# Kernel tuning notes

Hardware: AMD Instinct MI355X
Metric: run time of the kernel (lower is better)

Reference implementation:

```python
import jax, jax.numpy as jnp
import numpy as np

HIDDEN = 4096
N_HEADS = 32
N_KV_HEADS = 8
HEAD_DIM = HIDDEN // N_HEADS  # 128
ROPE_THETA = 10000.0
NEG_INF = -1e9


def rotate_half(x):
    x1, x2 = jnp.split(x, 2, axis=-1)
    return jnp.concatenate([-x2, x1], axis=-1)


def rope_cos_sin(seq_len, dim, dtype):
    inv_freq = 1.0 / (ROPE_THETA ** (jnp.arange(0, dim, 2, dtype=jnp.float32) / dim))
    t = jnp.arange(seq_len, dtype=jnp.float32)
    freqs = jnp.outer(t, inv_freq)              # (S, dim/2)
    emb = jnp.concatenate([freqs, freqs], -1)   # (S, dim)
    return jnp.cos(emb).astype(dtype), jnp.sin(emb).astype(dtype)


def setup_inputs() -> dict:
    key = jax.random.key(0)
    ks = jax.random.split(key, 5)
    B, S = 2, 2048
    hidden_states = jax.random.normal(ks[0], (B, S, HIDDEN), jnp.float32)
    # additive causal mask (B, 1, S, S)
    causal = jnp.triu(jnp.full((S, S), NEG_INF, jnp.float32), k=1)
    attention_mask = jnp.broadcast_to(causal[None, None], (B, 1, S, S))
    scale = 0.02
    wq = jax.random.normal(ks[1], (HIDDEN, HIDDEN), jnp.float32) * scale
    wk = jax.random.normal(ks[2], (N_KV_HEADS * HEAD_DIM, HIDDEN), jnp.float32) * scale
    wv = jax.random.normal(ks[3], (N_KV_HEADS * HEAD_DIM, HIDDEN), jnp.float32) * scale
    wo = jax.random.normal(ks[4], (HIDDEN, HIDDEN), jnp.float32) * scale
    return {"hidden_states": hidden_states, "attention_mask": attention_mask,
            "wq": wq, "wk": wk, "wv": wv, "wo": wo}


def reference(hidden_states, attention_mask, wq, wk, wv, wo):
    B, S, _ = hidden_states.shape
    H, Hk, D = N_HEADS, N_KV_HEADS, HEAD_DIM
    G = H // Hk  # kv groups

    q = (hidden_states @ wq.T).reshape(B, S, H, D).transpose(0, 2, 1, 3)   # (B,H,S,D)
    k = (hidden_states @ wk.T).reshape(B, S, Hk, D).transpose(0, 2, 1, 3)  # (B,Hk,S,D)
    v = (hidden_states @ wv.T).reshape(B, S, Hk, D).transpose(0, 2, 1, 3)

    cos, sin = rope_cos_sin(S, D, hidden_states.dtype)  # (S,D)
    cos = cos[None, None]  # (1,1,S,D)
    sin = sin[None, None]
    q = q * cos + rotate_half(q) * sin
    k = k * cos + rotate_half(k) * sin

    # GQA without materializing repeated K/V: view q as (B,Hk,G,S,D)
    qg = q.reshape(B, Hk, G, S, D)
    scores = jnp.einsum('bkgqd,bkld->bkgql', qg, k) / jnp.sqrt(jnp.asarray(D, q.dtype))
    scores = scores + attention_mask[:, :, None]  # (B,1,1,S,S) broadcast
    attn = jax.nn.softmax(scores.astype(jnp.float32), axis=-1).astype(q.dtype)
    out = jnp.einsum('bkgql,bkld->bkgqd', attn, v)  # (B,Hk,G,S,D)
    out = out.reshape(B, H, S, D).transpose(0, 2, 1, 3).reshape(B, S, H * D)
    return out @ wo.T
```

## Files before the change

### kernel.cpp

```cpp
#include <hip/hip_runtime.h>
#include <hip/hip_bf16.h>
#include <stdint.h>


#define HIDDEN 4096
#define NH 32
#define NKV 8
#define HD 128
#define SLEN 2048
#define BATCH 2
#define QKVLD 6144

typedef __attribute__((ext_vector_type(8))) short bf16x8;
typedef __attribute__((ext_vector_type(4))) float f32x4;

__device__ __forceinline__ unsigned short f2bf(float f) {
  __hip_bfloat16 h = __float2bfloat16(f);
  return *reinterpret_cast<unsigned short*>(&h);
}
__device__ __forceinline__ float bf2f(unsigned short h) {
  union { uint32_t u; float f; } v; v.u = ((uint32_t)h) << 16;
  return v.f;
}
__device__ __forceinline__ void gload_lds16(const void* g, void* l) {
  __builtin_amdgcn_global_load_lds(
      (const __attribute__((address_space(1))) unsigned int*)g,
      (__attribute__((address_space(3))) unsigned int*)l, 16, 0, 0);
}

__global__ __launch_bounds__(256) void cvt_f32_bf16(const float* __restrict__ in,
                                                    unsigned short* __restrict__ out) {
  size_t i = ((size_t)blockIdx.x * 256 + threadIdx.x) * 8;
  f32x4 a = *(const f32x4*)&in[i];
  f32x4 b = *(const f32x4*)&in[i + 4];
  bf16x8 o;
#pragma unroll
  for (int j = 0; j < 4; ++j) { o[j] = (short)f2bf(a[j]); o[4 + j] = (short)f2bf(b[j]); }
  *(bf16x8*)&out[i] = o;
}

__device__ __forceinline__ void store_out(unsigned short* C, size_t i, float v) { C[i] = f2bf(v); }
__device__ __forceinline__ void store_out(float* C, size_t i, float v) { C[i] = v; }

template <typename OutT>
__global__ __launch_bounds__(512, 2)
void gemm_bt256(const unsigned short* __restrict__ A, const unsigned short* __restrict__ B,
                OutT* __restrict__ C, int M, int N, int K) {
  __shared__ __align__(16) unsigned short lds[4 * 2048 * 8];

  const int tid = threadIdx.x;
  const int lane = tid & 63, w = tid >> 6;
  const int lr = lane & 15, lg = lane >> 4;
  const int wr = w >> 2, wc = w & 3;

  const int nbn = N >> 8;
  const int nwg = gridDim.x;
  int wg = (int)blockIdx.x;
  wg = (wg & 7) * (nwg >> 3) + (wg >> 3);
  const int bm = wg / nbn, bn = wg % nbn;

  const unsigned short* Ab = A + (size_t)bm * 256 * K;
  const unsigned short* Bb = B + (size_t)bn * 256 * K;

  f32x4 acc[8][4] = {};

  auto stage = [&](int t2) {
    const int kt = t2 * 32;
    unsigned short* lb = lds + (size_t)(t2 & 3) * 2048 * 8;
#pragma unroll
    for (int j = 0; j < 2; ++j) {
      int idx = tid + j * 512;
      gload_lds16(Ab + (size_t)(idx >> 2) * K + kt + (idx & 3) * 8,
                  lb + (size_t)(w * 64 + j * 512) * 8);
    }
#pragma unroll
    for (int j = 0; j < 2; ++j) {
      int idx = tid + j * 512;
      gload_lds16(Bb + (size_t)(idx >> 2) * K + kt + (idx & 3) * 8,
                  lb + (size_t)(1024 + w * 64 + j * 512) * 8);
    }
  };

  const int NT = K >> 5;

  stage(0);
  stage(1);
  stage(2);
  asm volatile("s_waitcnt vmcnt(8)" ::: "memory");
  __builtin_amdgcn_s_barrier();
  asm volatile("" ::: "memory");

#pragma unroll 1
  for (int t = 0; t < NT; ++t) {
    if (t + 3 < NT) stage(t + 3);

    const unsigned short* bufp = lds + (size_t)(t & 3) * 2048 * 8;
    bf16x8 af[8], bfv[4];
#pragma unroll
    for (int mi = 0; mi < 8; ++mi)
      af[mi] = *(const bf16x8*)&bufp[(size_t)(wr * 512 + mi * 64 + lr * 4 + lg) * 8];
#pragma unroll
    for (int ni = 0; ni < 4; ++ni)
      bfv[ni] = *(const bf16x8*)&bufp[(size_t)(1024 + wc * 256 + ni * 64 + lr * 4 + lg) * 8];

    __builtin_amdgcn_s_setprio(1);
#pragma unroll
    for (int mi = 0; mi < 8; ++mi)
#pragma unroll
      for (int ni = 0; ni < 4; ++ni)
        acc[mi][ni] = __builtin_amdgcn_mfma_f32_16x16x32_bf16(af[mi], bfv[ni], acc[mi][ni], 0, 0, 0);
    __builtin_amdgcn_s_setprio(0);

    if (t + 1 < NT) {
      if (t + 3 < NT)      asm volatile("s_waitcnt vmcnt(8)" ::: "memory");
      else if (t + 2 < NT) asm volatile("s_waitcnt vmcnt(4)" ::: "memory");
      else                 asm volatile("s_waitcnt vmcnt(0)" ::: "memory");
      __builtin_amdgcn_s_barrier();
      asm volatile("" ::: "memory");
    }
  }

#pragma unroll
  for (int mi = 0; mi < 8; ++mi)
#pragma unroll
    for (int ni = 0; ni < 4; ++ni)
#pragma unroll
      for (int r = 0; r < 4; ++r) {
        size_t row = (size_t)bm * 256 + wr * 128 + mi * 16 + lg * 4 + r;
        size_t col = (size_t)bn * 256 + wc * 64 + ni * 16 + lr;
        store_out(C, row * N + col, acc[mi][ni][r]);
      }
}

__global__ __launch_bounds__(256) void rope_tables(float* __restrict__ ct, float* __restrict__ st) {
  int idx = blockIdx.x * 256 + threadIdx.x;
  int s = idx >> 6, j = idx & 63;
  float inv = exp2f(-(float)j * (13.287712379549449f / 64.f));
  float f = (float)s * inv;
  ct[idx] = cosf(f);
  st[idx] = sinf(f);
}

__global__ __launch_bounds__(256) void rope_apply(unsigned short* __restrict__ X, int ld,
                                                  const float* __restrict__ ct,
                                                  const float* __restrict__ st, int heads) {
  int idx = blockIdx.x * 256 + threadIdx.x;
  int jc = (idx & 7) * 8;
  int t2 = idx >> 3;
  int hh = t2 % heads;
  int row = t2 / heads;
  int s = row & (SLEN - 1);
  unsigned short* p = X + (size_t)row * ld + hh * HD;
  bf16x8 lo = *(bf16x8*)&p[jc];
  bf16x8 hi = *(bf16x8*)&p[64 + jc];
  bf16x8 nlo, nhi;
#pragma unroll
  for (int j = 0; j < 8; ++j) {
    float c = ct[s * 64 + jc + j];
    float sn = st[s * 64 + jc + j];
    float xl = bf2f((unsigned short)(lo[j]));
    float xh = bf2f((unsigned short)(hi[j]));
    nlo[j] = (short)f2bf(xl * c - xh * sn);
    nhi[j] = (short)f2bf(xh * c + xl * sn);
  }
  *(bf16x8*)&p[jc] = nlo;
  *(bf16x8*)&p[64 + jc] = nhi;
}

__global__ __launch_bounds__(256) void transpose_v(const unsigned short* __restrict__ Vsrc, int ld,
                                                   unsigned short* __restrict__ VT) {
  __shared__ unsigned short tile[64][66];
  const int t = threadIdx.x;
  const int bs = blockIdx.x;
  const int bd = blockIdx.y;
  const int b = bs >> 5;
  const int s0 = (bs & 31) * 64;
  const int d0 = bd * 64;
#pragma unroll
  for (int it = 0; it < 2; ++it) {
    int si = (t >> 3) + it * 32;
    int dj = (t & 7) * 8;
    bf16x8 v = *(const bf16x8*)&Vsrc[(size_t)(b * SLEN + s0 + si) * ld + d0 + dj];
#pragma unroll
    for (int j = 0; j < 8; ++j) tile[si][dj + j] = (unsigned short)(v[j]);
  }
  __syncthreads();
#pragma unroll
  for (int it = 0; it < 2; ++it) {
    int di = (t >> 3) + it * 32;
    int sj = (t & 7) * 8;
    bf16x8 o;
#pragma unroll
    for (int j = 0; j < 8; ++j) o[j] = (short)tile[sj + j][di];
    int c = d0 + di;
    int kvh = c >> 7, d = c & 127;
    *(bf16x8*)&VT[(((size_t)b * NKV + kvh) * HD + d) * SLEN + s0 + sj] = o;
  }
}

__global__ __launch_bounds__(256, 2)
void attn_fwd(const unsigned short* __restrict__ QKV, const unsigned short* __restrict__ VTm,
              unsigned short* __restrict__ Om) {
  const int blk = blockIdx.x;
  const int xcd = blk & 7, jj = blk >> 3;
  const int g = xcd + ((jj >> 5) << 3);
  const int pair = jj & 31;
  const int kvh = g & 7, b = g >> 3;
  const int tid = threadIdx.x;
  const int lane = tid & 63, w = tid >> 6;
  const int lr = lane & 15, lg = lane >> 4;
  const int h = kvh * 4 + w;

  __shared__ __align__(16) unsigned short Ksm[64 * 136];
  __shared__ __align__(16) unsigned short Vsm[128 * 72];
  __shared__ __align__(16) unsigned short Psm[4][32 * 72];
  __shared__ float Alds[4][32];

  const float SL2E = 0.1275378504229740f;

  const unsigned short* Kb0 = QKV + (size_t)(b * SLEN) * QKVLD + 4096 + kvh * HD;
  const unsigned short* VTb = VTm + ((size_t)(b * NKV + kvh) * HD) * SLEN;

#pragma unroll 1
  for (int halfq = 0; halfq < 2; ++halfq) {
    const int qt = halfq ? (63 - pair) : pair;
    const int q0 = qt * 32;
    const int ntiles = (qt >> 1) + 1;

    bf16x8 qf[2][4];
    const unsigned short* Qb = QKV + (size_t)(b * SLEN + q0) * QKVLD + h * HD;
#pragma unroll
    for (int ni = 0; ni < 2; ++ni)
#pragma unroll
      for (int kd = 0; kd < 4; ++kd)
        qf[ni][kd] = *(const bf16x8*)&Qb[(size_t)(ni * 16 + lr) * QKVLD + kd * 32 + lg * 8];

    f32x4 acc_o[2][8] = {};
    float m_run[2] = {-1e30f, -1e30f};
    float l_run[2] = {0.f, 0.f};

    bf16x8 kreg[4], vreg[4];
#pragma unroll
    for (int i = 0; i < 4; ++i) {
      int c = tid + i * 256;
      kreg[i] = *(const bf16x8*)&Kb0[(size_t)(c >> 4) * QKVLD + (c & 15) * 8];
      vreg[i] = *(const bf16x8*)&VTb[(size_t)(c >> 3) * SLEN + (c & 7) * 8];
    }

#pragma unroll 1
    for (int t = 0; t < ntiles; ++t) {
      const int kv0 = t * 64;
      __syncthreads();
#pragma unroll
      for (int i = 0; i < 4; ++i) {
        int c = tid + i * 256;
        *(bf16x8*)&Ksm[(c >> 4) * 136 + (c & 15) * 8] = kreg[i];
        *(bf16x8*)&Vsm[(c >> 3) * 72 + (c & 7) * 8] = vreg[i];
      }
      __syncthreads();

      if (t + 1 < ntiles) {
#pragma unroll
        for (int i = 0; i < 4; ++i) {
          int c = tid + i * 256;
          kreg[i] = *(const bf16x8*)&Kb0[(size_t)(kv0 + 64 + (c >> 4)) * QKVLD + (c & 15) * 8];
          vreg[i] = *(const bf16x8*)&VTb[(size_t)(c >> 3) * SLEN + kv0 + 64 + (c & 7) * 8];
        }
      }

      f32x4 accs[4][2] = {};
#pragma unroll
      for (int kd = 0; kd < 4; ++kd) {
        bf16x8 kf[4];
#pragma unroll
        for (int mi = 0; mi < 4; ++mi)
          kf[mi] = *(const bf16x8*)&Ksm[(mi * 16 + lr) * 136 + kd * 32 + lg * 8];
        __builtin_amdgcn_s_setprio(1);
#pragma unroll
        for (int mi = 0; mi < 4; ++mi)
#pragma unroll
          for (int ni = 0; ni < 2; ++ni)
            accs[mi][ni] =
                __builtin_amdgcn_mfma_f32_16x16x32_bf16(kf[mi], qf[ni][kd], accs[mi][ni], 0, 0, 0);
        __builtin_amdgcn_s_setprio(0);
      }

      const bool domask = (t == ntiles - 1);
      float alpha[2];
#pragma unroll
      for (int ni = 0; ni < 2; ++ni) {
        float cmax = -1e30f;
#pragma unroll
        for (int mi = 0; mi < 4; ++mi)
#pragma unroll
          for (int r = 0; r < 4; ++r) {
            float s = accs[mi][ni][r] * SL2E;
            if (domask) {
              int key = kv0 + mi * 16 + lg * 4 + r;
              int qq = q0 + ni * 16 + lr;
              if (key > qq) s = -1e30f;
            }
            accs[mi][ni][r] = s;
            cmax = fmaxf(cmax, s);
          }
        cmax = fmaxf(cmax, __shfl_xor(cmax, 16));
        cmax = fmaxf(cmax, __shfl_xor(cmax, 32));
        float mnew = fmaxf(m_run[ni], cmax);
        alpha[ni] = exp2f(m_run[ni] - mnew);
        float psum = 0.f;
#pragma unroll
        for (int mi = 0; mi < 4; ++mi)
#pragma unroll
          for (int r = 0; r < 4; ++r) {
            float p = exp2f(accs[mi][ni][r] - mnew);
            accs[mi][ni][r] = p;
            psum += p;
          }
        psum += __shfl_xor(psum, 16);
        psum += __shfl_xor(psum, 32);
        l_run[ni] = l_run[ni] * alpha[ni] + psum;
        m_run[ni] = mnew;
      }

      if (__any(alpha[0] < 1.f) || __any(alpha[1] < 1.f)) {
        if (lg == 0) { Alds[w][lr] = alpha[0]; Alds[w][16 + lr] = alpha[1]; }
        f32x4 al0 = *(const f32x4*)&Alds[w][lg * 4];
        f32x4 al1 = *(const f32x4*)&Alds[w][16 + lg * 4];
#pragma unroll
        for (int nd = 0; nd < 8; ++nd)
#pragma unroll
          for (int r = 0; r < 4; ++r) {
            acc_o[0][nd][r] *= al0[r];
            acc_o[1][nd][r] *= al1[r];
          }
      }

#pragma unroll
      for (int ni = 0; ni < 2; ++ni)
#pragma unroll
        for (int mi = 0; mi < 4; ++mi)
#pragma unroll
          for (int rp = 0; rp < 4; rp += 2) {
            uint32_t pk = (uint32_t)f2bf(accs[mi][ni][rp]) |
                          ((uint32_t)f2bf(accs[mi][ni][rp + 1]) << 16);
            *(uint32_t*)&Psm[w][(ni * 16 + lr) * 72 + mi * 16 + lg * 4 + rp] = pk;
          }

#pragma unroll
      for (int ks = 0; ks < 2; ++ks) {
        bf16x8 pa[2];
#pragma unroll
        for (int pm = 0; pm < 2; ++pm)
          pa[pm] = *(const bf16x8*)&Psm[w][(pm * 16 + lr) * 72 + ks * 32 + lg * 8];
        __builtin_amdgcn_s_setprio(1);
#pragma unroll
        for (int nd = 0; nd < 8; ++nd) {
          bf16x8 vb = *(const bf16x8*)&Vsm[(nd * 16 + lr) * 72 + ks * 32 + lg * 8];
#pragma unroll
          for (int pm = 0; pm < 2; ++pm)
            acc_o[pm][nd] =
                __builtin_amdgcn_mfma_f32_16x16x32_bf16(pa[pm], vb, acc_o[pm][nd], 0, 0, 0);
        }
        __builtin_amdgcn_s_setprio(0);
      }
    }

    if (lg == 0) {
      Alds[w][lr] = 1.f / l_run[0];
      Alds[w][16 + lr] = 1.f / l_run[1];
    }
    f32x4 li0 = *(const f32x4*)&Alds[w][lg * 4];
    f32x4 li1 = *(const f32x4*)&Alds[w][16 + lg * 4];
    unsigned short* Ob = Om + ((size_t)(b * SLEN + q0) * NH + h) * HD;
#pragma unroll
    for (int pm = 0; pm < 2; ++pm)
#pragma unroll
      for (int nd = 0; nd < 8; ++nd)
#pragma unroll
        for (int r = 0; r < 4; ++r) {
          int qq = pm * 16 + lg * 4 + r;
          float v = acc_o[pm][nd][r] * (pm ? li1[r] : li0[r]);
          Ob[(size_t)qq * (NH * HD) + nd * 16 + lr] = f2bf(v);
        }
  }
}

extern "C" void kernel_launch(void* const* d_in, const int* in_sizes, int n_in,
                              void* d_out, int out_size, void* d_ws, size_t ws_size,
                              hipStream_t stream) {
  const float* hidden = (const float*)d_in[0];
  const float* wq = (const float*)d_in[2];
  const float* wk = (const float*)d_in[3];
  const float* wv = (const float*)d_in[4];
  const float* wo = (const float*)d_in[5];

  char* ws = (char*)d_ws;
  const size_t MB = 1ull << 20;
  unsigned short* Xbf  = (unsigned short*)(ws);
  unsigned short* Wqkv = (unsigned short*)(ws + 32 * MB);
  unsigned short* QKV  = (unsigned short*)(ws + 80 * MB);
  unsigned short* Ob   = (unsigned short*)(ws + 128 * MB);
  unsigned short* VTb  = (unsigned short*)(ws + 160 * MB);
  float* ct = (float*)(ws + 168 * MB);
  float* st = (float*)(ws + 168 * MB + 524288);

  cvt_f32_bf16<<<8192, 256, 0, stream>>>(hidden, Xbf);
  cvt_f32_bf16<<<8192, 256, 0, stream>>>(wq, Wqkv);
  cvt_f32_bf16<<<2048, 256, 0, stream>>>(wk, Wqkv + (size_t)4096 * 4096);
  cvt_f32_bf16<<<2048, 256, 0, stream>>>(wv, Wqkv + (size_t)5120 * 4096);

  gemm_bt256<unsigned short><<<384, 512, 0, stream>>>(Xbf, Wqkv, QKV, 4096, 6144, 4096);

  rope_tables<<<512, 256, 0, stream>>>(ct, st);
  rope_apply<<<4096, 256, 0, stream>>>(QKV, QKVLD, ct, st, NH);
  rope_apply<<<1024, 256, 0, stream>>>(QKV + 4096, QKVLD, ct, st, NKV);

  transpose_v<<<dim3(64, 16), 256, 0, stream>>>(QKV + 5120, QKVLD, VTb);

  attn_fwd<<<512, 256, 0, stream>>>(QKV, VTb, Ob);

  cvt_f32_bf16<<<8192, 256, 0, stream>>>(wo, Wqkv);
  gemm_bt256<float><<<256, 512, 0, stream>>>(Ob, Wqkv, (float*)d_out, 4096, 4096, 4096);
}
```

Measured before the change: 601.1 us.

## Restructure GEMM main loop into four interleaved phases with swizzled double-buffered LDS

Rewrites the 256x256 bf16 GEMM main loop to use 64-wide K tiles in two LDS buffers, split into four phases that each issue LDS reads, one half-tile global prefetch and 16 MFMAs, separated by barriers. It also XOR-swizzles the LDS column layout to reduce bank conflicts on fragment reads. The goal is better overlap of global loads, LDS reads and MFMA work, and lower register pressure from holding fewer A fragments at once. The cost is more barriers per iteration and a more fragile vmcnt accounting scheme.

```diff
diff --git a/kernel.cpp b/kernel.cpp
--- a/kernel.cpp
+++ b/kernel.cpp
@@ -46,12 +46,13 @@
 __global__ __launch_bounds__(512, 2)
 void gemm_bt256(const unsigned short* __restrict__ A, const unsigned short* __restrict__ B,
                 OutT* __restrict__ C, int M, int N, int K) {
-  __shared__ __align__(16) unsigned short lds[4 * 2048 * 8];
+  __shared__ __align__(16) unsigned short lds[2 * 4096 * 8];
 
   const int tid = threadIdx.x;
   const int lane = tid & 63, w = tid >> 6;
   const int lr = lane & 15, lg = lane >> 4;
   const int wr = w >> 2, wc = w & 3;
+  const int rsw = (lr >> 1) & 3;
 
   const int nbn = N >> 8;
   const int nwg = gridDim.x;
@@ -64,60 +65,87 @@
 
   f32x4 acc[8][4] = {};
 
-  auto stage = [&](int t2) {
-    const int kt = t2 * 32;
-    unsigned short* lb = lds + (size_t)(t2 & 3) * 2048 * 8;
+  auto stage_half = [&](int isA, int ks, int tile) {
+    const unsigned short* gb = isA ? Ab : Bb;
+    const int rb = (tile & 1) * 4096 + (isA ? 0 : 2048) + ks * 1024;
+    const int kcol = tile * 64 + ks * 32;
 #pragma unroll
     for (int j = 0; j < 2; ++j) {
-      int idx = tid + j * 512;
-      gload_lds16(Ab + (size_t)(idx >> 2) * K + kt + (idx & 3) * 8,
-                  lb + (size_t)(w * 64 + j * 512) * 8);
-    }
-#pragma unroll
-    for (int j = 0; j < 2; ++j) {
-      int idx = tid + j * 512;
-      gload_lds16(Bb + (size_t)(idx >> 2) * K + kt + (idx & 3) * 8,
-                  lb + (size_t)(1024 + w * 64 + j * 512) * 8);
+      int L = tid + j * 512;
+      int row = L >> 2, cc = L & 3;
+      int scc = cc ^ ((row >> 1) & 3);
+      gload_lds16(gb + (size_t)row * K + kcol + scc * 8, lds + (size_t)(rb + L) * 8);
     }
   };
-
-  const int NT = K >> 5;
-
-  stage(0);
-  stage(1);
-  stage(2);
-  asm volatile("s_waitcnt vmcnt(8)" ::: "memory");
+  auto read_a4 = [&](bf16x8* dst, int ks, int mi0, int p) {
+#pragma unroll
+    for (int i = 0; i < 4; ++i) {
+      int row = wr * 128 + (mi0 + i) * 16 + lr;
+      dst[i] = *(const bf16x8*)&lds[(size_t)(p * 4096 + ks * 1024 + row * 4 + (lg ^ rsw)) * 8];
+    }
+  };
+  auto read_b4 = [&](bf16x8* dst, int ks, int p) {
+#pragma unroll
+    for (int i = 0; i < 4; ++i) {
+      int row = wc * 64 + i * 16 + lr;
+      dst[i] =
+          *(const bf16x8*)&lds[(size_t)(p * 4096 + 2048 + ks * 1024 + row * 4 + (lg ^ rsw)) * 8];
+    }
+  };
+
+#define PHASE_SYNC()                                    \
+  __builtin_amdgcn_s_barrier();                         \
+  asm volatile("s_waitcnt lgkmcnt(0)" ::: "memory");    \
+  __builtin_amdgcn_sched_barrier(0)
+
+#define MFMA16(afq, bq, mb)                                                                   \
+  __builtin_amdgcn_s_setprio(1);                                                              \
+  _Pragma("unroll") for (int i_ = 0; i_ < 4; ++i_) _Pragma("unroll") for (int n_ = 0; n_ < 4; \
+                                                                          ++n_) acc[mb + i_]  \
+      [n_] = __builtin_amdgcn_mfma_f32_16x16x32_bf16(afq[i_], bq[n_], acc[mb + i_][n_], 0, 0, 0); \
+  __builtin_amdgcn_s_setprio(0);                                                              \
+  __builtin_amdgcn_s_barrier()
+
+  const int NT = K >> 6;
+
+  stage_half(1, 0, 0); stage_half(0, 0, 0); stage_half(1, 1, 0); stage_half(0, 1, 0);
+  if (NT > 1) { stage_half(0, 0, 1); stage_half(1, 0, 1); stage_half(0, 1, 1); }
+  if (NT > 1) asm volatile("s_waitcnt vmcnt(6)" ::: "memory");
+  else        asm volatile("s_waitcnt vmcnt(0)" ::: "memory");
   __builtin_amdgcn_s_barrier();
   asm volatile("" ::: "memory");
 
 #pragma unroll 1
   for (int t = 0; t < NT; ++t) {
-    if (t + 3 < NT) stage(t + 3);
-
-    const unsigned short* bufp = lds + (size_t)(t & 3) * 2048 * 8;
-    bf16x8 af[8], bfv[4];
-#pragma unroll
-    for (int mi = 0; mi < 8; ++mi)
-      af[mi] = *(const bf16x8*)&bufp[(size_t)(wr * 512 + mi * 64 + lr * 4 + lg) * 8];
-#pragma unroll
-    for (int ni = 0; ni < 4; ++ni)
-      bfv[ni] = *(const bf16x8*)&bufp[(size_t)(1024 + wc * 256 + ni * 64 + lr * 4 + lg) * 8];
-
-    __builtin_amdgcn_s_setprio(1);
-#pragma unroll
-    for (int mi = 0; mi < 8; ++mi)
-#pragma unroll
-      for (int ni = 0; ni < 4; ++ni)
-        acc[mi][ni] = __builtin_amdgcn_mfma_f32_16x16x32_bf16(af[mi], bfv[ni], acc[mi][ni], 0, 0, 0);
-    __builtin_amdgcn_s_setprio(0);
-
-    if (t + 1 < NT) {
-      if (t + 3 < NT)      asm volatile("s_waitcnt vmcnt(8)" ::: "memory");
-      else if (t + 2 < NT) asm volatile("s_waitcnt vmcnt(4)" ::: "memory");
-      else                 asm volatile("s_waitcnt vmcnt(0)" ::: "memory");
-      __builtin_amdgcn_s_barrier();
-      asm volatile("" ::: "memory");
-    }
+    const int p = t & 1;
+    bf16x8 afq[4], afq2[4], bq0[4], bq1[4];
+
+    read_a4(afq, 0, 0, p);
+    read_b4(bq0, 0, p);
+    if (t + 1 < NT) stage_half(1, 1, t + 1);
+    PHASE_SYNC();
+    MFMA16(afq, bq0, 0);
+
+    read_a4(afq2, 0, 4, p);
+    if (t + 2 < NT) stage_half(0, 0, t + 2);
+    PHASE_SYNC();
+    MFMA16(afq2, bq0, 4);
+
+    read_a4(afq, 1, 0, p);
+    read_b4(bq1, 1, p);
+    if (t + 2 < NT) stage_half(1, 0, t + 2);
+    PHASE_SYNC();
+    MFMA16(afq, bq1, 0);
+
+    read_a4(afq2, 1, 4, p);
+    if (t + 2 < NT) stage_half(0, 1, t + 2);
+    PHASE_SYNC();
+    MFMA16(afq2, bq1, 4);
+
+    if (t + 2 < NT)      asm volatile("s_waitcnt vmcnt(6)" ::: "memory");
+    else if (t + 1 < NT) asm volatile("s_waitcnt vmcnt(0)" ::: "memory");
+    __builtin_amdgcn_s_barrier();
+    asm volatile("" ::: "memory");
   }
 
 #pragma unroll
@@ -130,6 +158,8 @@
         size_t col = (size_t)bn * 256 + wc * 64 + ni * 16 + lr;
         store_out(C, row * N + col, acc[mi][ni][r]);
       }
+#undef PHASE_SYNC
+#undef MFMA16
 }
 
 __global__ __launch_bounds__(256) void rope_tables(float* __restrict__ ct, float* __restrict__ st) {
```

Measured after the change: 590.3 us. About the same (-1.8%).

## Restructure GEMM mainloop into 64-wide K tiles with phased double-buffered LDS pipeline

Applied to the files above, without the earlier changes.

Rewrites the bf16 GEMM main loop to use 64-wide K tiles in a two-buffer LDS layout. Each tile is split into four phases that interleave LDS reads, async global-to-LDS staging of later sub-tiles, and 16-MFMA groups, separated by barriers. An XOR swizzle on the LDS chunk index is added to reduce bank conflicts on fragment reads. The aim is finer overlap of memory and MFMA work, at the cost of more barriers per K step and more complex waitcnt bookkeeping.

```diff
diff --git a/kernel.cpp b/kernel.cpp
--- a/kernel.cpp
+++ b/kernel.cpp
@@ -46,12 +46,13 @@
 __global__ __launch_bounds__(512, 2)
 void gemm_bt256(const unsigned short* __restrict__ A, const unsigned short* __restrict__ B,
                 OutT* __restrict__ C, int M, int N, int K) {
-  __shared__ __align__(16) unsigned short lds[4 * 2048 * 8];
+  __shared__ __align__(16) unsigned short lds[2 * 4096 * 8];
 
   const int tid = threadIdx.x;
   const int lane = tid & 63, w = tid >> 6;
   const int lr = lane & 15, lg = lane >> 4;
   const int wr = w >> 2, wc = w & 3;
+  const int rsw = (lr >> 1) & 3;
 
   const int nbn = N >> 8;
   const int nwg = gridDim.x;
@@ -62,62 +63,97 @@
   const unsigned short* Ab = A + (size_t)bm * 256 * K;
   const unsigned short* Bb = B + (size_t)bn * 256 * K;
 
+  const int r0 = tid >> 2, s0 = (tid & 3) ^ ((tid >> 3) & 3);
+  const int L1 = tid + 512;
+  const int r1 = L1 >> 2, s1 = (L1 & 3) ^ ((L1 >> 3) & 3);
+  const unsigned short* gA0 = Ab + (size_t)r0 * K + s0 * 8;
+  const unsigned short* gA1 = Ab + (size_t)r1 * K + s1 * 8;
+  const unsigned short* gB0 = Bb + (size_t)r0 * K + s0 * 8;
+  const unsigned short* gB1 = Bb + (size_t)r1 * K + s1 * 8;
+
+  const unsigned short* rdA0 = &lds[(size_t)(wr * 512 + lr * 4 + (lg ^ rsw)) * 8];
+  const unsigned short* rdA1 = rdA0 + 32768;
+  const unsigned short* rdB0 = &lds[(size_t)(2048 + wc * 256 + lr * 4 + (lg ^ rsw)) * 8];
+  const unsigned short* rdB1 = rdB0 + 32768;
+
   f32x4 acc[8][4] = {};
 
-  auto stage = [&](int t2) {
-    const int kt = t2 * 32;
-    unsigned short* lb = lds + (size_t)(t2 & 3) * 2048 * 8;
-#pragma unroll
-    for (int j = 0; j < 2; ++j) {
-      int idx = tid + j * 512;
-      gload_lds16(Ab + (size_t)(idx >> 2) * K + kt + (idx & 3) * 8,
-                  lb + (size_t)(w * 64 + j * 512) * 8);
-    }
-#pragma unroll
-    for (int j = 0; j < 2; ++j) {
-      int idx = tid + j * 512;
-      gload_lds16(Bb + (size_t)(idx >> 2) * K + kt + (idx & 3) * 8,
-                  lb + (size_t)(1024 + w * 64 + j * 512) * 8);
-    }
+  auto stageA = [&](int ks, int tile) {
+    unsigned short* d = &lds[(size_t)((tile & 1) * 4096 + ks * 1024 + tid) * 8];
+    const int off = tile * 64 + ks * 32;
+    gload_lds16(gA0 + off, d);
+    gload_lds16(gA1 + off, d + 4096);
   };
-
-  const int NT = K >> 5;
-
-  stage(0);
-  stage(1);
-  stage(2);
-  asm volatile("s_waitcnt vmcnt(8)" ::: "memory");
+  auto stageB = [&](int ks, int tile) {
+    unsigned short* d = &lds[(size_t)((tile & 1) * 4096 + 2048 + ks * 1024 + tid) * 8];
+    const int off = tile * 64 + ks * 32;
+    gload_lds16(gB0 + off, d);
+    gload_lds16(gB1 + off, d + 4096);
+  };
+
+  const int NT = K >> 6;
+
+#define PHASE_SYNC()                                  \
+  __builtin_amdgcn_s_barrier();                       \
+  asm volatile("s_waitcnt lgkmcnt(0)" ::: "memory");  \
+  __builtin_amdgcn_sched_barrier(0)
+
+#define MFMA16(afq, bq, mb)                                                       \
+  __builtin_amdgcn_s_setprio(1);                                                  \
+  _Pragma("unroll") for (int i_ = 0; i_ < 4; ++i_)                                \
+  _Pragma("unroll") for (int n_ = 0; n_ < 4; ++n_)                                \
+    acc[(mb) + i_][n_] = __builtin_amdgcn_mfma_f32_16x16x32_bf16(                 \
+        afq[i_], bq[n_], acc[(mb) + i_][n_], 0, 0, 0);                            \
+  __builtin_amdgcn_s_setprio(0)
+
+#define RD_A(dst, P, ks, mi0)                                                     \
+  _Pragma("unroll") for (int i_ = 0; i_ < 4; ++i_)                                \
+    dst[i_] = *(const bf16x8*)((P ? rdA1 : rdA0) + (ks) * 8192 + ((mi0) + i_) * 512)
+#define RD_B(dst, P, ks)                                                          \
+  _Pragma("unroll") for (int i_ = 0; i_ < 4; ++i_)                                \
+    dst[i_] = *(const bf16x8*)((P ? rdB1 : rdB0) + (ks) * 8192 + i_ * 512)
+
+#define TILE_BODY(P, t)                                                           \
+  {                                                                               \
+    bf16x8 a0[4], a1[4], b0[4], b1[4];                                            \
+                     \
+    RD_A(a0, P, 0, 0); RD_B(b0, P, 0);                                            \
+    if ((t) + 1 < NT) stageA(1, (t) + 1);                                         \
+    PHASE_SYNC();                                                                 \
+    MFMA16(a0, b0, 0);                                                            \
+    __builtin_amdgcn_s_barrier();                                                 \
+                            \
+    RD_A(a1, P, 0, 4);                                                            \
+    if ((t) + 2 < NT) stageB(0, (t) + 2);                                         \
+    PHASE_SYNC();                                                                 \
+    MFMA16(a1, b0, 4);                                                            \
+    __builtin_amdgcn_s_barrier();                                                 \
+                     \
+    RD_A(a0, P, 1, 0); RD_B(b1, P, 1);                                            \
+    if ((t) + 2 < NT) stageA(0, (t) + 2);                                         \
+    PHASE_SYNC();                                                                 \
+    MFMA16(a0, b1, 0);                                                            \
+    __builtin_amdgcn_s_barrier();                                                 \
+            \
+    RD_A(a1, P, 1, 4);                                                            \
+    if ((t) + 2 < NT) stageB(1, (t) + 2);                                         \
+    PHASE_SYNC();                                                                 \
+    MFMA16(a1, b1, 4);                                                            \
+    if ((t) + 2 < NT)      asm volatile("s_waitcnt vmcnt(6)" ::: "memory");       \
+    else if ((t) + 1 < NT) asm volatile("s_waitcnt vmcnt(0)" ::: "memory");       \
+    __builtin_amdgcn_s_barrier();                                                 \
+  }
+
+  stageA(0, 0); stageB(0, 0); stageA(1, 0); stageB(1, 0);
+  stageB(0, 1); stageA(0, 1); stageB(1, 1);
+  asm volatile("s_waitcnt vmcnt(6)" ::: "memory");
   __builtin_amdgcn_s_barrier();
   asm volatile("" ::: "memory");
 
 #pragma unroll 1
-  for (int t = 0; t < NT; ++t) {
-    if (t + 3 < NT) stage(t + 3);
-
-    const unsigned short* bufp = lds + (size_t)(t & 3) * 2048 * 8;
-    bf16x8 af[8], bfv[4];
-#pragma unroll
-    for (int mi = 0; mi < 8; ++mi)
-      af[mi] = *(const bf16x8*)&bufp[(size_t)(wr * 512 + mi * 64 + lr * 4 + lg) * 8];
-#pragma unroll
-    for (int ni = 0; ni < 4; ++ni)
-      bfv[ni] = *(const bf16x8*)&bufp[(size_t)(1024 + wc * 256 + ni * 64 + lr * 4 + lg) * 8];
-
-    __builtin_amdgcn_s_setprio(1);
-#pragma unroll
-    for (int mi = 0; mi < 8; ++mi)
-#pragma unroll
-      for (int ni = 0; ni < 4; ++ni)
-        acc[mi][ni] = __builtin_amdgcn_mfma_f32_16x16x32_bf16(af[mi], bfv[ni], acc[mi][ni], 0, 0, 0);
-    __builtin_amdgcn_s_setprio(0);
-
-    if (t + 1 < NT) {
-      if (t + 3 < NT)      asm volatile("s_waitcnt vmcnt(8)" ::: "memory");
-      else if (t + 2 < NT) asm volatile("s_waitcnt vmcnt(4)" ::: "memory");
-      else                 asm volatile("s_waitcnt vmcnt(0)" ::: "memory");
-      __builtin_amdgcn_s_barrier();
-      asm volatile("" ::: "memory");
-    }
+  for (int t = 0; t < NT; t += 2) {
+    TILE_BODY(0, t);
+    TILE_BODY(1, t + 1);
   }
 
 #pragma unroll
@@ -130,6 +166,11 @@
         size_t col = (size_t)bn * 256 + wc * 64 + ni * 16 + lr;
         store_out(C, row * N + col, acc[mi][ni][r]);
       }
+#undef PHASE_SYNC
+#undef MFMA16
+#undef RD_A
+#undef RD_B
+#undef TILE_BODY
 }
 
 __global__ __launch_bounds__(256) void rope_tables(float* __restrict__ ct, float* __restrict__ st) {
@@ -409,7 +450,7 @@
   cvt_f32_bf16<<<2048, 256, 0, stream>>>(wk, Wqkv + (size_t)4096 * 4096);
   cvt_f32_bf16<<<2048, 256, 0, stream>>>(wv, Wqkv + (size_t)5120 * 4096);
 
-  gemm_bt256<unsigned short><<<384, 512, 0, stream>>>(Xbf, Wqkv, QKV, 4096, 6144, 4096);
+  gemm_bt256<unsigned short><<<1536 / 4, 512, 0, stream>>>(Xbf, Wqkv, QKV, 4096, 6144, 4096);
 
   rope_tables<<<512, 256, 0, stream>>>(ct, st);
   rope_apply<<<4096, 256, 0, stream>>>(QKV, QKVLD, ct, st, NH);
```

New measurement: 575.5 us. 4.3% less time.

## Double-buffer LDS fragment reads, swizzle LDS layout in GEMM, and merge RoPE launches

Applied to the files above, without the earlier changes.

The GEMM main loop now reads the next k-tile's A/B fragments from LDS into a second register set while MFMAs run on the current set, with one barrier per iteration placed before the reads. The global-to-LDS staging uses an XOR swizzle on the 16-byte chunk index, and the fragment reads use a matching swizzle, to reduce LDS bank conflicts. Global addresses are precomputed outside the loop. The two RoPE launches for Q and K are merged into one kernel. The cost is higher register pressure from the doubled fragment registers under launch_bounds(512,2), and the loop assumes an even number of k-tiles.

```diff
diff --git a/kernel.cpp b/kernel.cpp
--- a/kernel.cpp
+++ b/kernel.cpp
@@ -52,6 +52,7 @@
   const int lane = tid & 63, w = tid >> 6;
   const int lr = lane & 15, lg = lane >> 4;
   const int wr = w >> 2, wc = w & 3;
+  const int rsw = (lr >> 1) & 3;
 
   const int nbn = N >> 8;
   const int nwg = gridDim.x;
@@ -62,62 +63,74 @@
   const unsigned short* Ab = A + (size_t)bm * 256 * K;
   const unsigned short* Bb = B + (size_t)bn * 256 * K;
 
+  const int r0 = tid >> 2, s0 = (tid & 3) ^ ((tid >> 3) & 3);
+  const int L1 = tid + 512;
+  const int r1 = L1 >> 2, s1 = (L1 & 3) ^ ((L1 >> 3) & 3);
+  const unsigned short* gA0 = Ab + (size_t)r0 * K + s0 * 8;
+  const unsigned short* gA1 = Ab + (size_t)r1 * K + s1 * 8;
+  const unsigned short* gB0 = Bb + (size_t)r0 * K + s0 * 8;
+  const unsigned short* gB1 = Bb + (size_t)r1 * K + s1 * 8;
+
+  const unsigned short* rdA = &lds[(size_t)(wr * 512 + lr * 4 + (lg ^ rsw)) * 8];
+  const unsigned short* rdB = &lds[(size_t)(1024 + wc * 256 + lr * 4 + (lg ^ rsw)) * 8];
+
   f32x4 acc[8][4] = {};
 
   auto stage = [&](int t2) {
-    const int kt = t2 * 32;
     unsigned short* lb = lds + (size_t)(t2 & 3) * 2048 * 8;
-#pragma unroll
-    for (int j = 0; j < 2; ++j) {
-      int idx = tid + j * 512;
-      gload_lds16(Ab + (size_t)(idx >> 2) * K + kt + (idx & 3) * 8,
-                  lb + (size_t)(w * 64 + j * 512) * 8);
-    }
-#pragma unroll
-    for (int j = 0; j < 2; ++j) {
-      int idx = tid + j * 512;
-      gload_lds16(Bb + (size_t)(idx >> 2) * K + kt + (idx & 3) * 8,
-                  lb + (size_t)(1024 + w * 64 + j * 512) * 8);
-    }
+    const int off = t2 * 32;
+    gload_lds16(gA0 + off, lb + (size_t)tid * 8);
+    gload_lds16(gA1 + off, lb + (size_t)(512 + tid) * 8);
+    gload_lds16(gB0 + off, lb + (size_t)(1024 + tid) * 8);
+    gload_lds16(gB1 + off, lb + (size_t)(1536 + tid) * 8);
   };
 
+#define READ12(af, bf, bsel)                                                      \
+  {                                                                               \
+    const unsigned short* pA_ = rdA + (size_t)(bsel)*16384;                       \
+    const unsigned short* pB_ = rdB + (size_t)(bsel)*16384;                       \
+    _Pragma("unroll") for (int mi_ = 0; mi_ < 8; ++mi_)                           \
+        af[mi_] = *(const bf16x8*)(pA_ + mi_ * 512);                              \
+    _Pragma("unroll") for (int ni_ = 0; ni_ < 4; ++ni_)                           \
+        bf[ni_] = *(const bf16x8*)(pB_ + ni_ * 512);                              \
+  }
+
+#define MFMA32(af, bf)                                                            \
+  __builtin_amdgcn_s_setprio(1);                                                  \
+  _Pragma("unroll") for (int mi_ = 0; mi_ < 8; ++mi_)                             \
+  _Pragma("unroll") for (int ni_ = 0; ni_ < 4; ++ni_)                             \
+      acc[mi_][ni_] = __builtin_amdgcn_mfma_f32_16x16x32_bf16(                    \
+          af[mi_], bf[ni_], acc[mi_][ni_], 0, 0, 0);                              \
+  __builtin_amdgcn_s_setprio(0)
+
+#define VMW(t)                                                                    \
+  if ((t) + 3 < NT)      asm volatile("s_waitcnt vmcnt(8)" ::: "memory");         \
+  else if ((t) + 2 < NT) asm volatile("s_waitcnt vmcnt(4)" ::: "memory");         \
+  else if ((t) + 1 < NT) asm volatile("s_waitcnt vmcnt(0)" ::: "memory")
+
+#define ITER(cur_a, cur_b, nxt_a, nxt_b, t)                                       \
+  {                                                                               \
+    if ((t) + 3 < NT) stage((t) + 3);                                             \
+    VMW(t);                                                                       \
+    __builtin_amdgcn_s_barrier();                                                 \
+    if ((t) + 1 < NT) READ12(nxt_a, nxt_b, ((t) + 1) & 3);                        \
+    MFMA32(cur_a, cur_b);                                                         \
+    asm volatile("s_waitcnt lgkmcnt(0)" ::: "memory");                            \
+  }
+
   const int NT = K >> 5;
 
-  stage(0);
-  stage(1);
-  stage(2);
+  bf16x8 afA[8], bfA[4], afB[8], bfB[4];
+
+  stage(0); stage(1); stage(2);
   asm volatile("s_waitcnt vmcnt(8)" ::: "memory");
   __builtin_amdgcn_s_barrier();
-  asm volatile("" ::: "memory");
+  READ12(afA, bfA, 0);
 
 #pragma unroll 1
-  for (int t = 0; t < NT; ++t) {
-    if (t + 3 < NT) stage(t + 3);
-
-    const unsigned short* bufp = lds + (size_t)(t & 3) * 2048 * 8;
-    bf16x8 af[8], bfv[4];
-#pragma unroll
-    for (int mi = 0; mi < 8; ++mi)
-      af[mi] = *(const bf16x8*)&bufp[(size_t)(wr * 512 + mi * 64 + lr * 4 + lg) * 8];
-#pragma unroll
-    for (int ni = 0; ni < 4; ++ni)
-      bfv[ni] = *(const bf16x8*)&bufp[(size_t)(1024 + wc * 256 + ni * 64 + lr * 4 + lg) * 8];
-
-    __builtin_amdgcn_s_setprio(1);
-#pragma unroll
-    for (int mi = 0; mi < 8; ++mi)
-#pragma unroll
-      for (int ni = 0; ni < 4; ++ni)
-        acc[mi][ni] = __builtin_amdgcn_mfma_f32_16x16x32_bf16(af[mi], bfv[ni], acc[mi][ni], 0, 0, 0);
-    __builtin_amdgcn_s_setprio(0);
-
-    if (t + 1 < NT) {
-      if (t + 3 < NT)      asm volatile("s_waitcnt vmcnt(8)" ::: "memory");
-      else if (t + 2 < NT) asm volatile("s_waitcnt vmcnt(4)" ::: "memory");
-      else                 asm volatile("s_waitcnt vmcnt(0)" ::: "memory");
-      __builtin_amdgcn_s_barrier();
-      asm volatile("" ::: "memory");
-    }
+  for (int t = 0; t < NT; t += 2) {
+    ITER(afA, bfA, afB, bfB, t);
+    ITER(afB, bfB, afA, bfA, t + 1);
   }
 
 #pragma unroll
@@ -130,6 +143,10 @@
         size_t col = (size_t)bn * 256 + wc * 64 + ni * 16 + lr;
         store_out(C, row * N + col, acc[mi][ni][r]);
       }
+#undef READ12
+#undef MFMA32
+#undef VMW
+#undef ITER
 }
 
 __global__ __launch_bounds__(256) void rope_tables(float* __restrict__ ct, float* __restrict__ st) {
@@ -141,10 +158,9 @@
   st[idx] = sinf(f);
 }
 
-__global__ __launch_bounds__(256) void rope_apply(unsigned short* __restrict__ X, int ld,
-                                                  const float* __restrict__ ct,
-                                                  const float* __restrict__ st, int heads) {
-  int idx = blockIdx.x * 256 + threadIdx.x;
+__device__ __forceinline__ void rope_body(unsigned short* __restrict__ X, int ld,
+                                          const float* __restrict__ ct,
+                                          const float* __restrict__ st, int heads, int idx) {
   int jc = (idx & 7) * 8;
   int t2 = idx >> 3;
   int hh = t2 % heads;
@@ -165,6 +181,17 @@
   }
   *(bf16x8*)&p[jc] = nlo;
   *(bf16x8*)&p[64 + jc] = nhi;
+}
+
+__global__ __launch_bounds__(256) void rope_apply_qk(unsigned short* __restrict__ QKV,
+                                                     const float* __restrict__ ct,
+                                                     const float* __restrict__ st) {
+  int bid = blockIdx.x;
+  if (bid < 4096) {
+    rope_body(QKV, QKVLD, ct, st, NH, bid * 256 + threadIdx.x);
+  } else {
+    rope_body(QKV + 4096, QKVLD, ct, st, NKV, (bid - 4096) * 256 + threadIdx.x);
+  }
 }
 
 __global__ __launch_bounds__(256) void transpose_v(const unsigned short* __restrict__ Vsrc, int ld,
@@ -412,8 +439,7 @@
   gemm_bt256<unsigned short><<<384, 512, 0, stream>>>(Xbf, Wqkv, QKV, 4096, 6144, 4096);
 
   rope_tables<<<512, 256, 0, stream>>>(ct, st);
-  rope_apply<<<4096, 256, 0, stream>>>(QKV, QKVLD, ct, st, NH);
-  rope_apply<<<1024, 256, 0, stream>>>(QKV + 4096, QKVLD, ct, st, NKV);
+  rope_apply_qk<<<5120, 256, 0, stream>>>(QKV, ct, st);
 
   transpose_v<<<dim3(64, 16), 256, 0, stream>>>(QKV + 5120, QKVLD, VTb);
 
```

After: 572.3 us. -4.8%, faster.
